# Performance work log

Hardware: AMD Instinct MI355X
Metric: run time of the kernel (lower is better)

The kernel has to match this reference:

```python
import jax, jax.numpy as jnp
import numpy as np

BN_EPS = 1e-5

def _bn(y, g, b, m, v):
    # inference-mode BatchNorm2d over channel axis 1
    return (y - m[:, None, None]) * (g[:, None, None] / jnp.sqrt(v[:, None, None] + BN_EPS)) + b[:, None, None]

def setup_inputs() -> dict:
    key = jax.random.key(0)
    ks = jax.random.split(key, 16)
    B, C, H, W = 16, 128, 128, 128
    E, O = 256, 128
    inp = {
        'x1': jax.random.normal(ks[0], (B, C, H, W), jnp.float32),
        'x2': jax.random.normal(ks[1], (B, C, H, W), jnp.float32),
        # conv1: 1x1 Conv2d(C -> E)
        'w1': jax.random.normal(ks[2], (E, C), jnp.float32) * (1.0 / np.sqrt(C)),
        'b1': jax.random.normal(ks[3], (E,), jnp.float32) * 0.01,
        'g1': jax.random.uniform(ks[4], (E,), jnp.float32, 0.5, 1.5),
        'beta1': jax.random.normal(ks[5], (E,), jnp.float32) * 0.01,
        'm1': jax.random.normal(ks[6], (E,), jnp.float32) * 0.01,
        'v1': jax.random.uniform(ks[7], (E,), jnp.float32, 0.5, 1.5),
        # conv2: 1x1 Conv2d(E -> O)
        'w2': jax.random.normal(ks[8], (O, E), jnp.float32) * (1.0 / np.sqrt(E)),
        'b2': jax.random.normal(ks[9], (O,), jnp.float32) * 0.01,
        'g2': jax.random.uniform(ks[10], (O,), jnp.float32, 0.5, 1.5),
        'beta2': jax.random.normal(ks[11], (O,), jnp.float32) * 0.01,
        'm2': jax.random.normal(ks[12], (O,), jnp.float32) * 0.01,
        'v2': jax.random.uniform(ks[13], (O,), jnp.float32, 0.5, 1.5),
    }
    return inp

def _fft_atten(t, w1, b1, g1, beta1, m1, v1, w2, b2, g2, beta2, m2, v2):
    y = jnp.einsum('bchw,ec->behw', t, w1) + b1[:, None, None]
    y = jax.nn.relu(_bn(y, g1, beta1, m1, v1))
    y = jnp.einsum('behw,oe->bohw', y, w2) + b2[:, None, None]
    return _bn(y, g2, beta2, m2, v2)

def reference(x1, x2, w1, b1, g1, beta1, m1, v1, w2, b2, g2, beta2, m2, v2):
    b, c, h, w = x2.shape
    R = (h + w) // 32
    # vectorized high-pass mask (replaces the per-pixel Python loop)
    yy = (jnp.arange(h, dtype=x2.dtype) - (h - 1) / 2.0) ** 2
    xx = (jnp.arange(w, dtype=x2.dtype) - (w - 1) / 2.0) ** 2
    hpf = (yy[:, None] + xx[None, :] >= float(R * R)).astype(x2.dtype)  # [h,w]
    f = jnp.fft.fftn(x2, axes=(2, 3), norm='ortho')
    f = jnp.fft.fftshift(f)  # torch default shifts ALL axes, incl. batch/channel
    hf = f * hpf
    real = hf.real + _fft_atten(hf.real, w1, b1, g1, beta1, m1, v1, w2, b2, g2, beta2, m2, v2)
    imag = hf.imag + _fft_atten(hf.imag, w1, b1, g1, beta1, m1, v1, w2, b2, g2, beta2, m2, v2)
    hx = jnp.abs(jnp.fft.ifftn(jax.lax.complex(real, imag), s=x1.shape[-2:], axes=(2, 3), norm='ortho'))
    return (x1 * hx + x1, x2 * hx + x2, hx)
```

## Files before the change

### kernel.cpp

```cpp
#include <hip/hip_runtime.h>
#include <math.h>

#define PLANE 16384
#define NTOT  33554432u
#define TP    136
typedef unsigned int  uint;
typedef unsigned short ushort;

typedef __attribute__((ext_vector_type(8))) short  short8;
typedef __attribute__((ext_vector_type(8))) ushort ushort8;
typedef __attribute__((ext_vector_type(4))) ushort bf16x4;
typedef __attribute__((ext_vector_type(4))) uint   u32x4;
typedef __attribute__((ext_vector_type(4))) float  f32x4;

__device__ __forceinline__ ushort f2bf(float x){
  unsigned u = __float_as_uint(x);
  u = (u + 0x7FFFu + ((u >> 16) & 1u)) >> 16;
  return (ushort)u;
}
__device__ __forceinline__ float bf2f(ushort h){
  return __uint_as_float(((uint)h) << 16);
}
__device__ __forceinline__ uint pk(float a, float b){
  return (uint)f2bf(a) | ((uint)f2bf(b) << 16);
}

template<int SGN>
__device__ __forceinline__ void gen_table(ushort* Fre, ushort* Fim, int t){
  int n = t >> 2, kb = (t & 3) * 32;
  #pragma unroll
  for(int q=0; q<4; q++){
    ushort8 cv, sv;
    #pragma unroll
    for(int j=0; j<8; j++){
      int k = kb + q*8 + j;
      int idx = (n*k) & 127;
      float ss, cc;
      __sincosf((float)idx * 0.049087385212340517f, &ss, &cc);
      cv[j] = f2bf(cc);
      sv[j] = f2bf(SGN < 0 ? -ss : ss);
    }
    *(ushort8*)(&Fre[n*TP + kb + q*8]) = cv;
    *(ushort8*)(&Fim[n*TP + kb + q*8]) = sv;
  }
}

__global__ __launch_bounds__(256) void k_prep(
    const float* __restrict__ w1, const float* __restrict__ b1,
    const float* __restrict__ g1, const float* __restrict__ be1,
    const float* __restrict__ m1, const float* __restrict__ v1,
    const float* __restrict__ w2, const float* __restrict__ b2,
    const float* __restrict__ g2, const float* __restrict__ be2,
    const float* __restrict__ m2, const float* __restrict__ v2,
    float* __restrict__ wb){
  int g = blockIdx.x*256 + threadIdx.x;
  ushort* wbs = (ushort*)wb;
  if(g < 32768){
    int kt = (g >> 9) & 3, l = (g >> 3) & 63, j = g & 7;
    int et = g >> 11;
    int c = kt*32 + 8*(l>>4) + j;
    int e = et*16 + (l&15);
    float s1 = g1[e]*rsqrtf(v1[e]+1e-5f);
    wbs[g] = f2bf(w1[e*128 + c]*s1);
  } else {
    int g2i = g - 32768;
    int ot = g2i >> 12, kt = (g2i >> 9) & 7, l = (g2i >> 3) & 63, j = g2i & 7;
    int o = ot*16 + (l&15);
    int e = kt*32 + 8*(l>>4) + j;
    float s2 = g2[o]*rsqrtf(v2[o]+1e-5f);
    wbs[32768 + g2i] = f2bf(w2[o*256 + e]*s2);
  }
  if(g < 256){
    float s1 = g1[g]*rsqrtf(v1[g]+1e-5f);
    wb[32768 + g] = b1[g]*s1 + be1[g] - m1[g]*s1;
  }
  if(g < 128){
    float s2 = g2[g]*rsqrtf(v2[g]+1e-5f);
    wb[33024 + g] = b2[g]*s2 + be2[g] - m2[g]*s2;
  }
}

__global__ __launch_bounds__(512,1) void k_fft_fwd(const float* __restrict__ x2,
                                                   uint* __restrict__ spec){
  __shared__ ushort Fre[128*TP], Fim[128*TP];
  __shared__ ushort Pre[128*TP], Pim[128*TP];
  __shared__ ushort xb[2][16*TP];
  int t = threadIdx.x, l = t & 63, wv = t >> 6;
  int bid = blockIdx.x, b = bid >> 7, c = bid & 127;
  const float* src = x2 + (size_t)(b*128 + c)*PLANE;
  gen_table<-1>(Fre, Fim, t);
  int hr = t >> 5, c4 = (t & 31)*4;
  {
    f32x4 v = *(const f32x4*)(src + hr*128 + c4);
    bf16x4 o;
    #pragma unroll
    for(int j=0;j<4;j++) o[j] = f2bf(v[j]);
    *(bf16x4*)(&xb[0][hr*TP + c4]) = o;
  }
  __syncthreads();
  int koff = 8*(l >> 4);
  for(int s=0; s<8; s++){
    f32x4 pf;
    if(s < 7) pf = *(const f32x4*)(src + (16*(s+1) + hr)*128 + c4);
    int arow = (l & 15)*TP;
    int brow = (16*(wv ^ 4) + (l & 15))*TP;
    f32x4 pr = {0,0,0,0}, pi = {0,0,0,0};
    #pragma unroll
    for(int kt=0; kt<4; kt++){
      short8 xa = *(const short8*)(&xb[s&1][arow + kt*32 + koff]);
      short8 fr = *(const short8*)(&Fre[brow + kt*32 + koff]);
      short8 fi = *(const short8*)(&Fim[brow + kt*32 + koff]);
      pr = __builtin_amdgcn_mfma_f32_16x16x32_bf16(xa, fr, pr, 0,0,0);
      pi = __builtin_amdgcn_mfma_f32_16x16x32_bf16(xa, fi, pi, 0,0,0);
    }
    int wd = 16*wv + (l & 15);
    int hb = 16*s + 4*(l >> 4);
    bf16x4 pr4, pi4;
    #pragma unroll
    for(int r=0;r<4;r++){ pr4[r] = f2bf(pr[r]); pi4[r] = f2bf(pi[r]); }
    *(bf16x4*)(&Pre[wd*TP + hb]) = pr4;
    *(bf16x4*)(&Pim[wd*TP + hb]) = pi4;
    if(s < 7){
      bf16x4 o;
      #pragma unroll
      for(int j=0;j<4;j++) o[j] = f2bf(pf[j]);
      *(bf16x4*)(&xb[(s+1)&1][hr*TP + c4]) = o;
    }
    __syncthreads();
  }
  int bp = (b + 8) & 15, cp = (c + 64) & 127;
  uint* dst = spec + (size_t)(bp*128 + cp)*PLANE;
  int arow2 = (16*wv + (l & 15))*TP;
  short8 ar[4], ai[4];
  #pragma unroll
  for(int kt=0; kt<4; kt++){
    ar[kt] = *(const short8*)(&Pre[arow2 + kt*32 + koff]);
    ai[kt] = *(const short8*)(&Pim[arow2 + kt*32 + koff]);
  }
  const float SC = 1.0f/128.0f;
  uint* tw = ((uint*)xb) + wv*256;
  #pragma unroll
  for(int ct=0; ct<8; ct++){
    int brow = (16*(ct ^ 4) + (l & 15))*TP;
    f32x4 sr_ = {0,0,0,0}, si_ = {0,0,0,0};
    #pragma unroll
    for(int kt=0; kt<4; kt++){
      short8 fi = *(const short8*)(&Fim[brow + kt*32 + koff]);
      sr_ = __builtin_amdgcn_mfma_f32_16x16x32_bf16(ai[kt], fi, sr_, 0,0,0);
      si_ = __builtin_amdgcn_mfma_f32_16x16x32_bf16(ar[kt], fi, si_, 0,0,0);
    }
    sr_ = -sr_;
    #pragma unroll
    for(int kt=0; kt<4; kt++){
      short8 fr = *(const short8*)(&Fre[brow + kt*32 + koff]);
      sr_ = __builtin_amdgcn_mfma_f32_16x16x32_bf16(ar[kt], fr, sr_, 0,0,0);
      si_ = __builtin_amdgcn_mfma_f32_16x16x32_bf16(ai[kt], fr, si_, 0,0,0);
    }
    int hd0 = 16*ct;
    {
      int hd = hd0 + (l & 15);
      float dh = (float)hd - 63.5f;
      float dh2 = dh*dh;
      #pragma unroll
      for(int r=0; r<4; r++){
        int wd = 16*wv + 4*(l>>4) + r;
        float dw = (float)wd - 63.5f;
        float m = (dw*dw + dh2 >= 64.0f) ? SC : 0.0f;
        tw[(4*(l>>4)+r)*16 + (l&15)] = pk(sr_[r]*m, si_[r]*m);
      }
    }
    u32x4 v4 = *(u32x4*)(tw + (l>>2)*16 + (l&3)*4);
    *(u32x4*)(dst + (16*wv + (l>>2))*128 + hd0 + (l&3)*4) = v4;
  }
}

#define XPITCH 136
#define EPITCH 264
__global__ __launch_bounds__(256,3) void k_conv(const float* __restrict__ wb,
                                                const uint* __restrict__ spec,
                                                uint* __restrict__ zo){
  __shared__ ushort xs[64*XPITCH];
  __shared__ ushort hs[64*EPITCH];
  const ushort* wbs = (const ushort*)wb;
  int bid = blockIdx.x;
  int b = bid >> 9;
  int pix0 = (bid & 511) * 32;
  const uint* sp = spec + (size_t)(b*128)*PLANE + pix0;
  int t = threadIdx.x, l = t & 63, w = t >> 6;
  {
    int p = t & 31, g = t >> 5;
    #pragma unroll
    for(int half=0; half<2; half++){
      ushort re8[8], im8[8];
      #pragma unroll
      for(int k=0;k<8;k++){
        uint u = sp[(size_t)(g*16 + half*8 + k)*PLANE + p];
        re8[k] = (ushort)u; im8[k] = (ushort)(u>>16);
      }
      *(ushort8*)(xs + p*XPITCH      + g*16 + half*8) = *(ushort8*)re8;
      *(ushort8*)(xs + (p+32)*XPITCH + g*16 + half*8) = *(ushort8*)im8;
    }
  }
  short8 bw1[4][4];
  #pragma unroll
  for(int et=0; et<4; et++)
    #pragma unroll
    for(int kt=0; kt<4; kt++)
      bw1[et][kt] = *(const short8*)(wbs + (((w*4+et)*4 + kt)*64 + l)*8);
  float c1v[4];
  #pragma unroll
  for(int et=0; et<4; et++) c1v[et] = wb[32768 + w*64 + et*16 + (l&15)];
  __syncthreads();
  #pragma unroll
  for(int mt=0; mt<4; mt++){
    short8 xa[4];
    #pragma unroll
    for(int kt=0; kt<4; kt++)
      xa[kt] = *(const short8*)(xs + (mt*16 + (l&15))*XPITCH + kt*32 + 8*(l>>4));
    f32x4 a0 = {0,0,0,0}, a1 = {0,0,0,0}, a2 = {0,0,0,0}, a3 = {0,0,0,0};
    #pragma unroll
    for(int kt=0; kt<4; kt++){
      a0 = __builtin_amdgcn_mfma_f32_16x16x32_bf16(xa[kt], bw1[0][kt], a0, 0,0,0);
      a1 = __builtin_amdgcn_mfma_f32_16x16x32_bf16(xa[kt], bw1[1][kt], a1, 0,0,0);
      a2 = __builtin_amdgcn_mfma_f32_16x16x32_bf16(xa[kt], bw1[2][kt], a2, 0,0,0);
      a3 = __builtin_amdgcn_mfma_f32_16x16x32_bf16(xa[kt], bw1[3][kt], a3, 0,0,0);
    }
    #pragma unroll
    for(int et=0; et<4; et++){
      f32x4 av = et==0?a0 : et==1?a1 : et==2?a2 : a3;
      #pragma unroll
      for(int r=0; r<4; r++){
        float h = fmaxf(av[r] + c1v[et], 0.f);
        hs[(mt*16 + (l>>4)*4 + r)*EPITCH + w*64 + et*16 + (l&15)] = f2bf(h);
      }
    }
  }
  short8 aw2[2][8];
  #pragma unroll
  for(int ot=0; ot<2; ot++)
    #pragma unroll
    for(int kt=0; kt<8; kt++)
      aw2[ot][kt] = *(const short8*)(wbs + 32768 + (((w*2+ot)*8 + kt)*64 + l)*8);
  float c2r[8];
  #pragma unroll
  for(int ot=0; ot<2; ot++)
    #pragma unroll
    for(int r=0; r<4; r++)
      c2r[ot*4+r] = wb[33024 + w*32 + ot*16 + (l>>4)*4 + r];
  __syncthreads();
  f32x4 d[2][4];
  #pragma unroll
  for(int ot=0; ot<2; ot++)
    #pragma unroll
    for(int pt=0; pt<4; pt++) d[ot][pt] = (f32x4){0,0,0,0};
  for(int kt=0; kt<8; kt++){
    short8 hb[4];
    #pragma unroll
    for(int pt=0; pt<4; pt++)
      hb[pt] = *(const short8*)(hs + (pt*16 + (l&15))*EPITCH + kt*32 + 8*(l>>4));
    #pragma unroll
    for(int ot=0; ot<2; ot++)
      #pragma unroll
      for(int pt=0; pt<4; pt++)
        d[ot][pt] = __builtin_amdgcn_mfma_f32_16x16x32_bf16(aw2[ot][kt], hb[pt], d[ot][pt], 0,0,0);
  }
  uint* zb = zo + (size_t)(b*128)*PLANE + pix0;
  #pragma unroll
  for(int ot=0; ot<2; ot++){
    #pragma unroll
    for(int pp=0; pp<2; pp++){
      #pragma unroll
      for(int r=0; r<4; r++){
        int o = w*32 + ot*16 + (l>>4)*4 + r;
        int p = pp*16 + (l&15);
        float re = d[ot][pp][r]   + c2r[ot*4+r] + bf2f(xs[p*XPITCH + o]);
        float im = d[ot][pp+2][r] + c2r[ot*4+r] + bf2f(xs[(p+32)*XPITCH + o]);
        zb[(size_t)o*PLANE + p] = pk(re, im);
      }
    }
  }
}

__global__ __launch_bounds__(512,1) void k_ifft_out(const uint* z,
                                                    const float* __restrict__ xin1,
                                                    const float* __restrict__ xin2,
                                                    float* out){
  __shared__ ushort Gre[128*TP], Gim[128*TP];
  __shared__ ushort Tre[128*TP], Tim[128*TP];
  __shared__ ushort zbb[4][16*TP];
  int t = threadIdx.x, l = t & 63, wv = t >> 6;
  int bid = blockIdx.x, b = bid >> 7, o = bid & 127;
  size_t plane = (size_t)(b*128 + o)*PLANE;
  const uint* zp = z + plane;
  gen_table<1>(Gre, Gim, t);
  int rr = t >> 5, c4 = (t & 31)*4;
  {
    u32x4 u = *(const u32x4*)(zp + rr*128 + c4);
    bf16x4 ur, ui;
    #pragma unroll
    for(int j=0;j<4;j++){ ur[j] = (ushort)u[j]; ui[j] = (ushort)(u[j]>>16); }
    *(bf16x4*)(&zbb[0][rr*TP + c4]) = ur;
    *(bf16x4*)(&zbb[2][rr*TP + c4]) = ui;
  }
  __syncthreads();
  int koff = 8*(l >> 4);
  for(int s=0; s<8; s++){
    u32x4 pf;
    if(s < 7) pf = *(const u32x4*)(zp + (16*(s+1) + rr)*128 + c4);
    int arow = (l & 15)*TP;
    int brow = (16*wv + (l & 15))*TP;
    short8 zr[4], zi[4], gr[4], gi[4];
    #pragma unroll
    for(int kt=0; kt<4; kt++){
      zr[kt] = *(const short8*)(&zbb[s&1][arow + kt*32 + koff]);
      zi[kt] = *(const short8*)(&zbb[2+(s&1)][arow + kt*32 + koff]);
      gr[kt] = *(const short8*)(&Gre[brow + kt*32 + koff]);
      gi[kt] = *(const short8*)(&Gim[brow + kt*32 + koff]);
    }
    f32x4 tr = {0,0,0,0}, ti = {0,0,0,0};
    #pragma unroll
    for(int kt=0; kt<4; kt++) tr = __builtin_amdgcn_mfma_f32_16x16x32_bf16(zi[kt], gi[kt], tr, 0,0,0);
    tr = -tr;
    #pragma unroll
    for(int kt=0; kt<4; kt++) tr = __builtin_amdgcn_mfma_f32_16x16x32_bf16(zr[kt], gr[kt], tr, 0,0,0);
    #pragma unroll
    for(int kt=0; kt<4; kt++){
      ti = __builtin_amdgcn_mfma_f32_16x16x32_bf16(zr[kt], gi[kt], ti, 0,0,0);
      ti = __builtin_amdgcn_mfma_f32_16x16x32_bf16(zi[kt], gr[kt], ti, 0,0,0);
    }
    int nh = 16*wv + (l & 15);
    int wdb = 16*s + 4*(l >> 4);
    bf16x4 t4r, t4i;
    #pragma unroll
    for(int r=0;r<4;r++){ t4r[r] = f2bf(tr[r]); t4i[r] = f2bf(ti[r]); }
    *(bf16x4*)(&Tre[nh*TP + wdb]) = t4r;
    *(bf16x4*)(&Tim[nh*TP + wdb]) = t4i;
    if(s < 7){
      bf16x4 ur, ui;
      #pragma unroll
      for(int j=0;j<4;j++){ ur[j] = (ushort)pf[j]; ui[j] = (ushort)(pf[j]>>16); }
      *(bf16x4*)(&zbb[(s+1)&1][rr*TP + c4]) = ur;
      *(bf16x4*)(&zbb[2+((s+1)&1)][rr*TP + c4]) = ui;
    }
    __syncthreads();
  }
  int arow2 = (16*wv + (l & 15))*TP;
  short8 ar[4], ai[4];
  #pragma unroll
  for(int kt=0; kt<4; kt++){
    ar[kt] = *(const short8*)(&Tre[arow2 + kt*32 + koff]);
    ai[kt] = *(const short8*)(&Tim[arow2 + kt*32 + koff]);
  }
  const float SC = 1.0f/128.0f;
  float* hw = ((float*)zbb) + wv*320;
  #pragma unroll
  for(int ct=0; ct<8; ct++){
    int brow = (16*ct + (l & 15))*TP;
    f32x4 sr_ = {0,0,0,0}, si_ = {0,0,0,0};
    #pragma unroll
    for(int kt=0; kt<4; kt++){
      short8 gi = *(const short8*)(&Gim[brow + kt*32 + koff]);
      sr_ = __builtin_amdgcn_mfma_f32_16x16x32_bf16(ai[kt], gi, sr_, 0,0,0);
      si_ = __builtin_amdgcn_mfma_f32_16x16x32_bf16(ar[kt], gi, si_, 0,0,0);
    }
    sr_ = -sr_;
    #pragma unroll
    for(int kt=0; kt<4; kt++){
      short8 gr = *(const short8*)(&Gre[brow + kt*32 + koff]);
      sr_ = __builtin_amdgcn_mfma_f32_16x16x32_bf16(ar[kt], gr, sr_, 0,0,0);
      si_ = __builtin_amdgcn_mfma_f32_16x16x32_bf16(ai[kt], gr, si_, 0,0,0);
    }
    #pragma unroll
    for(int r=0; r<4; r++)
      hw[(4*(l>>4)+r)*20 + (l&15)] = sqrtf(sr_[r]*sr_[r] + si_[r]*si_[r]) * SC;
    f32x4 h4 = *(f32x4*)(hw + (l>>2)*20 + (l&3)*4);
    size_t idx4 = plane + (size_t)(16*wv + (l>>2))*128 + 16*ct + (l&3)*4;
    f32x4 u = *(const f32x4*)(xin1 + idx4);
    f32x4 v = *(const f32x4*)(xin2 + idx4);
    f32x4 o1, o2;
    #pragma unroll
    for(int j=0;j<4;j++){ o1[j] = u[j]*h4[j] + u[j]; o2[j] = v[j]*h4[j] + v[j]; }
    *(f32x4*)(out + idx4) = o1;
    *(f32x4*)(out + NTOT + idx4) = o2;
    *(f32x4*)(out + 2u*NTOT + idx4) = h4;
  }
}

extern "C" void kernel_launch(void* const* d_in, const int* in_sizes, int n_in,
                              void* d_out, int out_size, void* d_ws, size_t ws_size,
                              hipStream_t stream){
  (void)in_sizes; (void)n_in; (void)d_ws; (void)ws_size; (void)out_size;
  const float* x1  = (const float*)d_in[0];
  const float* x2  = (const float*)d_in[1];
  const float* w1  = (const float*)d_in[2];
  const float* b1  = (const float*)d_in[3];
  const float* g1  = (const float*)d_in[4];
  const float* be1 = (const float*)d_in[5];
  const float* m1  = (const float*)d_in[6];
  const float* v1  = (const float*)d_in[7];
  const float* w2  = (const float*)d_in[8];
  const float* b2  = (const float*)d_in[9];
  const float* g2  = (const float*)d_in[10];
  const float* be2 = (const float*)d_in[11];
  const float* m2  = (const float*)d_in[12];
  const float* v2  = (const float*)d_in[13];
  float* out = (float*)d_out;
  float* wb   = out;
  uint*  spec = (uint*)(out + NTOT);
  uint*  z    = (uint*)(out + 2u*NTOT);
  hipLaunchKernelGGL(k_prep,     dim3(256),  dim3(256), 0, stream,
                     w1,b1,g1,be1,m1,v1,w2,b2,g2,be2,m2,v2, wb);
  hipLaunchKernelGGL(k_fft_fwd,  dim3(2048), dim3(512), 0, stream, x2, spec);
  hipLaunchKernelGGL(k_conv,     dim3(8192), dim3(256), 0, stream, wb, spec, z);
  hipLaunchKernelGGL(k_ifft_out, dim3(2048), dim3(512), 0, stream, z, x1, x2, out);
}
```

Before: 436.0 us.

## Keep DFT twiddles in registers and read inputs directly to raise FFT occupancy

Both FFT kernels drop the 128x128 shared-memory twiddle tables. Each lane now generates its twiddle fragments in registers, and the second-stage DFT reuses a quarter-size fragment set through sign flips that follow DFT symmetry. The first stage reads global input straight into MFMA fragments, which removes the double-buffered staging and the per-step barriers. The smaller LDS footprint lets launch bounds go from 1 to 4 blocks per CU. The costs are more registers per thread, and uncoalesced, unprefetched global reads that now sit on the MFMA critical path.

```diff
diff --git a/kernel.cpp b/kernel.cpp
--- a/kernel.cpp
+++ b/kernel.cpp
@@ -24,26 +24,30 @@
 __device__ __forceinline__ uint pk(float a, float b){
   return (uint)f2bf(a) | ((uint)f2bf(b) << 16);
 }
-
-template<int SGN>
-__device__ __forceinline__ void gen_table(ushort* Fre, ushort* Fim, int t){
-  int n = t >> 2, kb = (t & 3) * 32;
-  #pragma unroll
-  for(int q=0; q<4; q++){
-    ushort8 cv, sv;
-    #pragma unroll
-    for(int j=0; j<8; j++){
-      int k = kb + q*8 + j;
-      int idx = (n*k) & 127;
-      float ss, cc;
-      __sincosf((float)idx * 0.049087385212340517f, &ss, &cc);
-      cv[j] = f2bf(cc);
-      sv[j] = f2bf(SGN < 0 ? -ss : ss);
-    }
-    *(ushort8*)(&Fre[n*TP + kb + q*8]) = cv;
-    *(ushort8*)(&Fim[n*TP + kb + q*8]) = sv;
-  }
-}
+__device__ __forceinline__ void unpack2(u32x4 a, u32x4 b, short8& re, short8& im){
+  union { uint u[4]; short8 s; } R, I;
+  R.u[0] = (a[0]&0xffffu) | (a[1]<<16);
+  R.u[1] = (a[2]&0xffffu) | (a[3]<<16);
+  R.u[2] = (b[0]&0xffffu) | (b[1]<<16);
+  R.u[3] = (b[2]&0xffffu) | (b[3]<<16);
+  I.u[0] = (a[0]>>16) | (a[1]&0xffff0000u);
+  I.u[1] = (a[2]>>16) | (a[3]&0xffff0000u);
+  I.u[2] = (b[0]>>16) | (b[1]&0xffff0000u);
+  I.u[3] = (b[2]>>16) | (b[3]&0xffff0000u);
+  re = R.s; im = I.s;
+}
+__device__ __forceinline__ short8 cvt8(f32x4 a, f32x4 b){
+  union { ushort h[8]; short8 s; } r;
+  #pragma unroll
+  for(int j=0;j<4;j++){ r.h[j]=f2bf(a[j]); r.h[4+j]=f2bf(b[j]); }
+  return r.s;
+}
+__device__ __forceinline__ short8 frg(short8 base, uint m){
+  union { short8 s; u32x4 u; } x; x.s = base;
+  x.u[0]^=m; x.u[1]^=m; x.u[2]^=m; x.u[3]^=m;
+  return x.s;
+}
+#define W128 0.049087385212340517f
 
 __global__ __launch_bounds__(256) void k_prep(
     const float* __restrict__ w1, const float* __restrict__ b1,
@@ -80,93 +84,95 @@
   }
 }
 
-__global__ __launch_bounds__(512,1) void k_fft_fwd(const float* __restrict__ x2,
+__global__ __launch_bounds__(512,4) void k_fft_fwd(const float* __restrict__ x2,
                                                    uint* __restrict__ spec){
-  __shared__ ushort Fre[128*TP], Fim[128*TP];
   __shared__ ushort Pre[128*TP], Pim[128*TP];
-  __shared__ ushort xb[2][16*TP];
-  int t = threadIdx.x, l = t & 63, wv = t >> 6;
-  int bid = blockIdx.x, b = bid >> 7, c = bid & 127;
-  const float* src = x2 + (size_t)(b*128 + c)*PLANE;
-  gen_table<-1>(Fre, Fim, t);
-  int hr = t >> 5, c4 = (t & 31)*4;
+  __shared__ ushort scr[8*640];
+  int t = threadIdx.x, l = t & 63, wv = t >> 6, c = l & 15, q = l >> 4;
+  int bid = blockIdx.x, b = bid >> 7, ch = bid & 127;
+  const float* src = x2 + (size_t)(b*128 + ch)*PLANE;
+  short8 fr[4], fi[4];
   {
-    f32x4 v = *(const f32x4*)(src + hr*128 + c4);
-    bf16x4 o;
-    #pragma unroll
-    for(int j=0;j<4;j++) o[j] = f2bf(v[j]);
-    *(bf16x4*)(&xb[0][hr*TP + c4]) = o;
-  }
-  __syncthreads();
-  int koff = 8*(l >> 4);
+    int n = 16*(wv^4) + c;
+    #pragma unroll
+    for(int kt=0; kt<4; kt++){
+      union{ushort h[8]; short8 s;} R, I;
+      #pragma unroll
+      for(int j=0;j<8;j++){
+        int k = kt*32 + 8*q + j;
+        float ss, cc; __sincosf((float)((n*k)&127)*W128, &ss, &cc);
+        R.h[j] = f2bf(cc); I.h[j] = f2bf(-ss);
+      }
+      fr[kt]=R.s; fi[kt]=I.s;
+    }
+  }
   for(int s=0; s<8; s++){
-    f32x4 pf;
-    if(s < 7) pf = *(const f32x4*)(src + (16*(s+1) + hr)*128 + c4);
-    int arow = (l & 15)*TP;
-    int brow = (16*(wv ^ 4) + (l & 15))*TP;
     f32x4 pr = {0,0,0,0}, pi = {0,0,0,0};
     #pragma unroll
     for(int kt=0; kt<4; kt++){
-      short8 xa = *(const short8*)(&xb[s&1][arow + kt*32 + koff]);
-      short8 fr = *(const short8*)(&Fre[brow + kt*32 + koff]);
-      short8 fi = *(const short8*)(&Fim[brow + kt*32 + koff]);
-      pr = __builtin_amdgcn_mfma_f32_16x16x32_bf16(xa, fr, pr, 0,0,0);
-      pi = __builtin_amdgcn_mfma_f32_16x16x32_bf16(xa, fi, pi, 0,0,0);
-    }
-    int wd = 16*wv + (l & 15);
-    int hb = 16*s + 4*(l >> 4);
-    bf16x4 pr4, pi4;
-    #pragma unroll
-    for(int r=0;r<4;r++){ pr4[r] = f2bf(pr[r]); pi4[r] = f2bf(pi[r]); }
-    *(bf16x4*)(&Pre[wd*TP + hb]) = pr4;
-    *(bf16x4*)(&Pim[wd*TP + hb]) = pi4;
-    if(s < 7){
-      bf16x4 o;
-      #pragma unroll
-      for(int j=0;j<4;j++) o[j] = f2bf(pf[j]);
-      *(bf16x4*)(&xb[(s+1)&1][hr*TP + c4]) = o;
-    }
-    __syncthreads();
-  }
-  int bp = (b + 8) & 15, cp = (c + 64) & 127;
+      const float* ap = src + (16*s + c)*128 + kt*32 + 8*q;
+      short8 xa = cvt8(*(const f32x4*)ap, *(const f32x4*)(ap+4));
+      pr = __builtin_amdgcn_mfma_f32_16x16x32_bf16(xa, fr[kt], pr, 0,0,0);
+      pi = __builtin_amdgcn_mfma_f32_16x16x32_bf16(xa, fi[kt], pi, 0,0,0);
+    }
+    bf16x4 p4r, p4i;
+    #pragma unroll
+    for(int r=0;r<4;r++){ p4r[r]=f2bf(pr[r]); p4i[r]=f2bf(pi[r]); }
+    *(bf16x4*)(&Pre[(16*wv+c)*TP + 16*s + 4*q]) = p4r;
+    *(bf16x4*)(&Pim[(16*wv+c)*TP + 16*s + 4*q]) = p4i;
+  }
+  short8 st_r[4][2], st_i[4][2];
+  #pragma unroll
+  for(int a=0;a<4;a++){
+    int n = 16*a + c;
+    #pragma unroll
+    for(int kk=0;kk<2;kk++){
+      union{ushort h[8]; short8 s;} R, I;
+      #pragma unroll
+      for(int j=0;j<8;j++){
+        int k = kk*32 + 8*q + j;
+        float ss, cc; __sincosf((float)((n*k)&127)*W128, &ss, &cc);
+        R.h[j] = f2bf(cc); I.h[j] = f2bf(-ss);
+      }
+      st_r[a][kk]=R.s; st_i[a][kk]=I.s;
+    }
+  }
+  short8 ar[4], ai[4];
+  #pragma unroll
+  for(int kt=0; kt<4; kt++){
+    ar[kt] = *(const short8*)(&Pre[(16*wv+c)*TP + kt*32 + 8*q]);
+    ai[kt] = *(const short8*)(&Pim[(16*wv+c)*TP + kt*32 + 8*q]);
+  }
+  int bp = (b + 8) & 15, cp = (ch + 64) & 127;
   uint* dst = spec + (size_t)(bp*128 + cp)*PLANE;
-  int arow2 = (16*wv + (l & 15))*TP;
-  short8 ar[4], ai[4];
-  #pragma unroll
-  for(int kt=0; kt<4; kt++){
-    ar[kt] = *(const short8*)(&Pre[arow2 + kt*32 + koff]);
-    ai[kt] = *(const short8*)(&Pim[arow2 + kt*32 + koff]);
-  }
   const float SC = 1.0f/128.0f;
-  uint* tw = ((uint*)xb) + wv*256;
+  uint LM = (c&1) ? 0x80008000u : 0u;
+  uint* tw = ((uint*)scr) + wv*320;
   #pragma unroll
   for(int ct=0; ct<8; ct++){
-    int brow = (16*(ct ^ 4) + (l & 15))*TP;
-    f32x4 sr_ = {0,0,0,0}, si_ = {0,0,0,0};
-    #pragma unroll
-    for(int kt=0; kt<4; kt++){
-      short8 fi = *(const short8*)(&Fim[brow + kt*32 + koff]);
-      sr_ = __builtin_amdgcn_mfma_f32_16x16x32_bf16(ai[kt], fi, sr_, 0,0,0);
-      si_ = __builtin_amdgcn_mfma_f32_16x16x32_bf16(ar[kt], fi, si_, 0,0,0);
-    }
-    sr_ = -sr_;
-    #pragma unroll
-    for(int kt=0; kt<4; kt++){
-      short8 fr = *(const short8*)(&Fre[brow + kt*32 + koff]);
-      sr_ = __builtin_amdgcn_mfma_f32_16x16x32_bf16(ar[kt], fr, sr_, 0,0,0);
-      si_ = __builtin_amdgcn_mfma_f32_16x16x32_bf16(ai[kt], fr, si_, 0,0,0);
+    const uint hiM = (ct<4) ? 0x80000000u : 0u;
+    f32x4 sp = {0,0,0,0}, sn = {0,0,0,0}, si = {0,0,0,0};
+    #pragma unroll
+    for(int kt=0; kt<4; kt++){
+      uint m = ((kt>=2)?LM:0u) ^ hiM;
+      short8 br = frg(st_r[ct&3][kt&1], m);
+      short8 bi = frg(st_i[ct&3][kt&1], m);
+      sp = __builtin_amdgcn_mfma_f32_16x16x32_bf16(ar[kt], br, sp, 0,0,0);
+      sn = __builtin_amdgcn_mfma_f32_16x16x32_bf16(ai[kt], bi, sn, 0,0,0);
+      si = __builtin_amdgcn_mfma_f32_16x16x32_bf16(ar[kt], bi, si, 0,0,0);
+      si = __builtin_amdgcn_mfma_f32_16x16x32_bf16(ai[kt], br, si, 0,0,0);
     }
     int hd0 = 16*ct;
     {
-      int hd = hd0 + (l & 15);
+      int hd = hd0 + c;
       float dh = (float)hd - 63.5f;
       float dh2 = dh*dh;
       #pragma unroll
       for(int r=0; r<4; r++){
-        int wd = 16*wv + 4*(l>>4) + r;
+        int wd = 16*wv + 4*q + r;
         float dw = (float)wd - 63.5f;
-        float m = (dw*dw + dh2 >= 64.0f) ? SC : 0.0f;
-        tw[(4*(l>>4)+r)*16 + (l&15)] = pk(sr_[r]*m, si_[r]*m);
+        float mm = (dw*dw + dh2 >= 64.0f) ? SC : 0.0f;
+        tw[(4*q+r)*16 + c] = pk((sp[r]-sn[r])*mm, si[r]*mm);
       }
     }
     u32x4 v4 = *(u32x4*)(tw + (l>>2)*16 + (l&3)*4);
@@ -281,98 +287,94 @@
   }
 }
 
-__global__ __launch_bounds__(512,1) void k_ifft_out(const uint* z,
+__global__ __launch_bounds__(512,4) void k_ifft_out(const uint* z,
                                                     const float* __restrict__ xin1,
                                                     const float* __restrict__ xin2,
                                                     float* out){
-  __shared__ ushort Gre[128*TP], Gim[128*TP];
   __shared__ ushort Tre[128*TP], Tim[128*TP];
-  __shared__ ushort zbb[4][16*TP];
-  int t = threadIdx.x, l = t & 63, wv = t >> 6;
+  __shared__ ushort scr[8*640];
+  int t = threadIdx.x, l = t & 63, wv = t >> 6, c = l & 15, q = l >> 4;
   int bid = blockIdx.x, b = bid >> 7, o = bid & 127;
   size_t plane = (size_t)(b*128 + o)*PLANE;
   const uint* zp = z + plane;
-  gen_table<1>(Gre, Gim, t);
-  int rr = t >> 5, c4 = (t & 31)*4;
+  short8 gr[4], gi[4];
   {
-    u32x4 u = *(const u32x4*)(zp + rr*128 + c4);
-    bf16x4 ur, ui;
-    #pragma unroll
-    for(int j=0;j<4;j++){ ur[j] = (ushort)u[j]; ui[j] = (ushort)(u[j]>>16); }
-    *(bf16x4*)(&zbb[0][rr*TP + c4]) = ur;
-    *(bf16x4*)(&zbb[2][rr*TP + c4]) = ui;
+    int n = 16*wv + c;
+    #pragma unroll
+    for(int kt=0; kt<4; kt++){
+      union{ushort h[8]; short8 s;} R, I;
+      #pragma unroll
+      for(int j=0;j<8;j++){
+        int k = kt*32 + 8*q + j;
+        float ss, cc; __sincosf((float)((n*k)&127)*W128, &ss, &cc);
+        R.h[j] = f2bf(cc); I.h[j] = f2bf(ss);
+      }
+      gr[kt]=R.s; gi[kt]=I.s;
+    }
+  }
+  for(int s=0; s<8; s++){
+    f32x4 tp = {0,0,0,0}, tn = {0,0,0,0}, ti = {0,0,0,0};
+    #pragma unroll
+    for(int kt=0; kt<4; kt++){
+      const uint* ap = zp + (16*s + c)*128 + kt*32 + 8*q;
+      short8 zr, zi;
+      unpack2(*(const u32x4*)ap, *(const u32x4*)(ap+4), zr, zi);
+      tp = __builtin_amdgcn_mfma_f32_16x16x32_bf16(zr, gr[kt], tp, 0,0,0);
+      tn = __builtin_amdgcn_mfma_f32_16x16x32_bf16(zi, gi[kt], tn, 0,0,0);
+      ti = __builtin_amdgcn_mfma_f32_16x16x32_bf16(zr, gi[kt], ti, 0,0,0);
+      ti = __builtin_amdgcn_mfma_f32_16x16x32_bf16(zi, gr[kt], ti, 0,0,0);
+    }
+    bf16x4 t4r, t4i;
+    #pragma unroll
+    for(int r=0;r<4;r++){ t4r[r]=f2bf(tp[r]-tn[r]); t4i[r]=f2bf(ti[r]); }
+    *(bf16x4*)(&Tre[(16*wv+c)*TP + 16*s + 4*q]) = t4r;
+    *(bf16x4*)(&Tim[(16*wv+c)*TP + 16*s + 4*q]) = t4i;
   }
   __syncthreads();
-  int koff = 8*(l >> 4);
-  for(int s=0; s<8; s++){
-    u32x4 pf;
-    if(s < 7) pf = *(const u32x4*)(zp + (16*(s+1) + rr)*128 + c4);
-    int arow = (l & 15)*TP;
-    int brow = (16*wv + (l & 15))*TP;
-    short8 zr[4], zi[4], gr[4], gi[4];
-    #pragma unroll
-    for(int kt=0; kt<4; kt++){
-      zr[kt] = *(const short8*)(&zbb[s&1][arow + kt*32 + koff]);
-      zi[kt] = *(const short8*)(&zbb[2+(s&1)][arow + kt*32 + koff]);
-      gr[kt] = *(const short8*)(&Gre[brow + kt*32 + koff]);
-      gi[kt] = *(const short8*)(&Gim[brow + kt*32 + koff]);
-    }
-    f32x4 tr = {0,0,0,0}, ti = {0,0,0,0};
-    #pragma unroll
-    for(int kt=0; kt<4; kt++) tr = __builtin_amdgcn_mfma_f32_16x16x32_bf16(zi[kt], gi[kt], tr, 0,0,0);
-    tr = -tr;
-    #pragma unroll
-    for(int kt=0; kt<4; kt++) tr = __builtin_amdgcn_mfma_f32_16x16x32_bf16(zr[kt], gr[kt], tr, 0,0,0);
-    #pragma unroll
-    for(int kt=0; kt<4; kt++){
-      ti = __builtin_amdgcn_mfma_f32_16x16x32_bf16(zr[kt], gi[kt], ti, 0,0,0);
-      ti = __builtin_amdgcn_mfma_f32_16x16x32_bf16(zi[kt], gr[kt], ti, 0,0,0);
-    }
-    int nh = 16*wv + (l & 15);
-    int wdb = 16*s + 4*(l >> 4);
-    bf16x4 t4r, t4i;
-    #pragma unroll
-    for(int r=0;r<4;r++){ t4r[r] = f2bf(tr[r]); t4i[r] = f2bf(ti[r]); }
-    *(bf16x4*)(&Tre[nh*TP + wdb]) = t4r;
-    *(bf16x4*)(&Tim[nh*TP + wdb]) = t4i;
-    if(s < 7){
-      bf16x4 ur, ui;
-      #pragma unroll
-      for(int j=0;j<4;j++){ ur[j] = (ushort)pf[j]; ui[j] = (ushort)(pf[j]>>16); }
-      *(bf16x4*)(&zbb[(s+1)&1][rr*TP + c4]) = ur;
-      *(bf16x4*)(&zbb[2+((s+1)&1)][rr*TP + c4]) = ui;
-    }
-    __syncthreads();
-  }
-  int arow2 = (16*wv + (l & 15))*TP;
+  short8 st_r[4][2], st_i[4][2];
+  #pragma unroll
+  for(int a=0;a<4;a++){
+    int n = 16*a + c;
+    #pragma unroll
+    for(int kk=0;kk<2;kk++){
+      union{ushort h[8]; short8 s;} R, I;
+      #pragma unroll
+      for(int j=0;j<8;j++){
+        int k = kk*32 + 8*q + j;
+        float ss, cc; __sincosf((float)((n*k)&127)*W128, &ss, &cc);
+        R.h[j] = f2bf(cc); I.h[j] = f2bf(ss);
+      }
+      st_r[a][kk]=R.s; st_i[a][kk]=I.s;
+    }
+  }
   short8 ar[4], ai[4];
   #pragma unroll
   for(int kt=0; kt<4; kt++){
-    ar[kt] = *(const short8*)(&Tre[arow2 + kt*32 + koff]);
-    ai[kt] = *(const short8*)(&Tim[arow2 + kt*32 + koff]);
+    ar[kt] = *(const short8*)(&Tre[(16*wv+c)*TP + kt*32 + 8*q]);
+    ai[kt] = *(const short8*)(&Tim[(16*wv+c)*TP + kt*32 + 8*q]);
   }
   const float SC = 1.0f/128.0f;
-  float* hw = ((float*)zbb) + wv*320;
+  uint LM = (c&1) ? 0x80008000u : 0u;
+  float* hw = ((float*)scr) + wv*320;
   #pragma unroll
   for(int ct=0; ct<8; ct++){
-    int brow = (16*ct + (l & 15))*TP;
-    f32x4 sr_ = {0,0,0,0}, si_ = {0,0,0,0};
-    #pragma unroll
-    for(int kt=0; kt<4; kt++){
-      short8 gi = *(const short8*)(&Gim[brow + kt*32 + koff]);
-      sr_ = __builtin_amdgcn_mfma_f32_16x16x32_bf16(ai[kt], gi, sr_, 0,0,0);
-      si_ = __builtin_amdgcn_mfma_f32_16x16x32_bf16(ar[kt], gi, si_, 0,0,0);
-    }
-    sr_ = -sr_;
-    #pragma unroll
-    for(int kt=0; kt<4; kt++){
-      short8 gr = *(const short8*)(&Gre[brow + kt*32 + koff]);
-      sr_ = __builtin_amdgcn_mfma_f32_16x16x32_bf16(ar[kt], gr, sr_, 0,0,0);
-      si_ = __builtin_amdgcn_mfma_f32_16x16x32_bf16(ai[kt], gr, si_, 0,0,0);
-    }
-    #pragma unroll
-    for(int r=0; r<4; r++)
-      hw[(4*(l>>4)+r)*20 + (l&15)] = sqrtf(sr_[r]*sr_[r] + si_[r]*si_[r]) * SC;
+    const uint hiM = (ct>=4) ? 0x80000000u : 0u;
+    f32x4 sp = {0,0,0,0}, sn = {0,0,0,0}, si = {0,0,0,0};
+    #pragma unroll
+    for(int kt=0; kt<4; kt++){
+      uint m = ((kt>=2)?LM:0u) ^ hiM;
+      short8 br = frg(st_r[ct&3][kt&1], m);
+      short8 bi = frg(st_i[ct&3][kt&1], m);
+      sp = __builtin_amdgcn_mfma_f32_16x16x32_bf16(ar[kt], br, sp, 0,0,0);
+      sn = __builtin_amdgcn_mfma_f32_16x16x32_bf16(ai[kt], bi, sn, 0,0,0);
+      si = __builtin_amdgcn_mfma_f32_16x16x32_bf16(ar[kt], bi, si, 0,0,0);
+      si = __builtin_amdgcn_mfma_f32_16x16x32_bf16(ai[kt], br, si, 0,0,0);
+    }
+    #pragma unroll
+    for(int r=0; r<4; r++){
+      float re = sp[r]-sn[r], im = si[r];
+      hw[(4*q+r)*20 + c] = sqrtf(re*re + im*im) * SC;
+    }
     f32x4 h4 = *(f32x4*)(hw + (l>>2)*20 + (l&3)*4);
     size_t idx4 = plane + (size_t)(16*wv + (l>>2))*128 + 16*ct + (l&3)*4;
     f32x4 u = *(const f32x4*)(xin1 + idx4);
```

After: 575.1 us. 1.32x slower.
